# Optimization experiments

Hardware: AMD Instinct MI355X
Metric: run time of the kernel (lower is better)

## Reference

```python
import jax, jax.numpy as jnp
from jax import lax
import numpy as np

B, S = 256, 512
VOCAB, EMB_D = 50000, 300
POS_MAX, POS_D = 512, 16
CNN_OUT, K, NCLASS = 50, 5, 10


def setup_inputs() -> dict:
    key = jax.random.key(0)
    ks = jax.random.split(key, 7)
    return {
        "tokens": jax.random.randint(ks[0], (B, S), 0, VOCAB),
        "embed_table": jax.random.normal(ks[1], (VOCAB, EMB_D), jnp.float32),
        "pos_table": jax.random.normal(ks[2], (POS_MAX, POS_D), jnp.float32),
        "conv_w": jax.random.normal(ks[3], (CNN_OUT, EMB_D + 2 * POS_D, K), jnp.float32) * 0.05,
        "conv_b": jax.random.normal(ks[4], (CNN_OUT,), jnp.float32) * 0.05,
        "fc_w": jax.random.normal(ks[5], (NCLASS, CNN_OUT), jnp.float32) * 0.1,
        "fc_b": jax.random.normal(ks[6], (NCLASS,), jnp.float32) * 0.1,
        "entity1": 1,
        "entity2": 2,
    }


def _nearest_entity_dist(tokens, entity, max_pos):
    # Distance from each token to the nearest occurrence of `entity`,
    # clipped to [0, max_pos-1]; sentences without the entity clip to max.
    Sl = tokens.shape[1]
    idx = jnp.arange(Sl)
    occ = tokens == entity  # [B, S]
    big = 2 * Sl
    # nearest occurrence index to the left (running max) and right (running min)
    left = lax.cummax(jnp.where(occ, idx, -big), axis=1)
    right = lax.cummin(jnp.where(occ, idx, big), axis=1, reverse=True)
    dist = jnp.minimum(idx - left, right - idx)
    return jnp.clip(dist, 0, max_pos - 1)


def reference(tokens, embed_table, pos_table, conv_w, conv_b, fc_w, fc_b,
              entity1, entity2):
    emb = embed_table[tokens]                      # [B, S, EMB_D] gather
    pad = jnp.all(emb == 0.0, axis=-1)             # [B, S] zero-row mask
    feats = [emb]
    for ent in (entity1, entity2):
        d = _nearest_entity_dist(tokens, ent, pos_table.shape[0])
        pe = pos_table[d]                          # [B, S, POS_D]
        pe = jnp.where(pad[..., None], 0.0, pe)    # zero masked positions
        feats.append(pe)
    x = jnp.concatenate(feats, axis=-1)            # [B, S, 332]
    x = jnp.transpose(x, (0, 2, 1))                # [B, C, S]
    pad_hw = conv_w.shape[-1] // 2
    y = lax.conv_general_dilated(
        x, conv_w, window_strides=(1,), padding=[(pad_hw, pad_hw)],
        dimension_numbers=("NCH", "OIH", "NCH"))
    y = jax.nn.relu(y + conv_b[None, :, None])     # [B, 50, S]
    y = jnp.max(y, axis=2)                         # full-length max pool -> [B, 50]
    out = y @ fc_w.T + fc_b                        # [B, NCLASS]
    return out
```

## Files before the change

kernel.cpp:

```cpp
#include <hip/hip_runtime.h>
#include <hip/hip_bf16.h>

typedef __attribute__((ext_vector_type(8))) short short8;
typedef __attribute__((ext_vector_type(4))) float floatx4;

#define BB 256
#define SS 512
#define VOCAB 50000
#define EMB_D 300
#define POS_MAX 512
#define POS_D 16
#define CNN_OUT 50
#define KW 5
#define NCLASS 10
#define C_IN 332
#define KS2 10
#define NB2 20
#define NWF2 (KS2 * NB2 * 64 * 8)
#define PSTR 320
#define ESTR 328
#define FSTR2 328
#define MROWS 64
#define FROWS 68
#define NB_PACK 225
#define NB_POSP 640
#define NB_DIST BB

__device__ __forceinline__ unsigned pack2bf(float x, float y) {
    __hip_bfloat162 h = __float22bfloat162_rn(make_float2(x, y));
    return *reinterpret_cast<unsigned*>(&h);
}

__device__ __forceinline__ unsigned short f2bf(float x) {
    unsigned u = __float_as_uint(x);
    u += 0x7FFF + ((u >> 16) & 1);
    return (unsigned short)(u >> 16);
}

__device__ __forceinline__ float bflo(unsigned u) { return __uint_as_float(u << 16); }
__device__ __forceinline__ float bfhi(unsigned u) { return __uint_as_float(u & 0xFFFF0000u); }

__device__ __forceinline__ unsigned comb(unsigned a, unsigned b, unsigned c,
                                         float sa, float sp) {
    float rlo = sa * bflo(a) + sp * (bflo(b) + bflo(c));
    float rhi = sa * bfhi(a) + sp * (bfhi(b) + bfhi(c));
    return pack2bf(rlo, rhi);
}

__global__ __launch_bounds__(512) void k_prep(const float* __restrict__ conv_w,
                                              const float* __restrict__ pos,
                                              unsigned short* __restrict__ Wf2,
                                              unsigned short* __restrict__ P1,
                                              unsigned short* __restrict__ P2,
                                              float* __restrict__ ymax,
                                              const int* __restrict__ tokens,
                                              const int* __restrict__ e1p,
                                              const int* __restrict__ e2p,
                                              int* __restrict__ d1,
                                              int* __restrict__ d2) {
    __shared__ int cnt1, cnt2;
    __shared__ int lst1[SS], lst2[SS];
    int bid = blockIdx.x, tid = threadIdx.x;
    if (bid < NB_PACK) {
        int idx = bid * 512 + tid;
        if (idx < NWF2) {
            int j = idx & 7, l = (idx >> 3) & 63;
            int rest = idx >> 9;
            int nb = rest % 20, ks = rest / 20;
            int c = ks * 32 + ((l >> 4) << 3) + j;
            int col = nb * 16 + (l & 15);
            int k = col >> 6, o = col & 63;
            float v = 0.f;
            if (c < EMB_D && o < CNN_OUT)
                v = conv_w[o * (C_IN * KW) + c * KW + k];
            Wf2[idx] = f2bf(v);
        } else if (idx < NWF2 + BB * CNN_OUT) {
            ymax[idx - NWF2] = 0.f;
        }
    } else if (bid < NB_PACK + NB_POSP) {
        int idx = (bid - NB_PACK) * 512 + tid;
        int tb = idx / (POS_MAX * PSTR);
        int r = idx % (POS_MAX * PSTR);
        int d = r / PSTR, col = r % PSTR;
        int k = col >> 6, o = col & 63;
        float v = 0.f;
        if (o < CNN_OUT) {
            const float* pr = pos + d * POS_D;
            const float* wb = conv_w + o * (C_IN * KW) + (EMB_D + tb * POS_D) * KW + k;
            #pragma unroll
            for (int c = 0; c < POS_D; ++c) v += pr[c] * wb[c * KW];
        }
        (tb ? P2 : P1)[d * PSTR + col] = f2bf(v);
    } else {
        int b = bid - NB_PACK - NB_POSP;
        int s = tid;
        if (s == 0) { cnt1 = 0; cnt2 = 0; }
        __syncthreads();
        int tok = tokens[b * SS + s];
        int e1 = *e1p, e2 = *e2p;
        if (tok == e1) lst1[atomicAdd(&cnt1, 1)] = s;
        if (tok == e2) lst2[atomicAdd(&cnt2, 1)] = s;
        __syncthreads();
        int dd1 = POS_MAX - 1;
        int n1 = cnt1;
        for (int i = 0; i < n1; ++i) dd1 = min(dd1, abs(s - lst1[i]));
        int dd2 = POS_MAX - 1;
        int n2 = cnt2;
        for (int i = 0; i < n2; ++i) dd2 = min(dd2, abs(s - lst2[i]));
        d1[b * SS + s] = dd1;
        d2[b * SS + s] = dd2;
    }
}

__global__ __launch_bounds__(256, 2) void k_proj(const float* __restrict__ E,
                                                 const unsigned short* __restrict__ Wf2,
                                                 unsigned short* __restrict__ P,
                                                 int* __restrict__ rowz) {
    __shared__ __align__(16) unsigned short Elds[64 * ESTR];
    int tid = threadIdx.x, lane = tid & 63, w = tid >> 6;
    int t0 = blockIdx.x * 64;

    int q = tid & 3, r = tid >> 2;
    int t = t0 + r;
    bool tv = (t < VOCAB);
    const float4* src = (const float4*)(E + (size_t)t * EMB_D);
    float4 v[19];
    #pragma unroll
    for (int i = 0; i < 19; ++i) {
        int c4 = q + i * 4;
        v[i] = (tv && c4 < 75) ? src[c4] : make_float4(0.f, 0.f, 0.f, 0.f);
    }
    bool nz = false;
    #pragma unroll
    for (int i = 0; i < 19; ++i)
        nz |= (v[i].x != 0.f) | (v[i].y != 0.f) | (v[i].z != 0.f) | (v[i].w != 0.f);
    #pragma unroll
    for (int i = 0; i < 19; ++i) {
        int c4 = q + i * 4;
        if (c4 < 75)
            *(uint2*)&Elds[r * ESTR + c4 * 4] =
                make_uint2(pack2bf(v[i].x, v[i].y), pack2bf(v[i].z, v[i].w));
    }
    {
        #pragma unroll
        for (int j = 0; j < 3; ++j) {
            int u = q * 3 + j;
            if (u < 10) *(unsigned*)&Elds[r * ESTR + 300 + u * 2] = 0u;
        }
    }
    {
        unsigned long long bal = __ballot(nz);
        int g = lane >> 2;
        if (q == 0 && tv) rowz[t] = (((bal >> (g * 4)) & 0xFULL) == 0ULL) ? 1 : 0;
    }
    __syncthreads();

    floatx4 acc[4][5];
    #pragma unroll
    for (int mm = 0; mm < 4; ++mm)
        #pragma unroll
        for (int nb = 0; nb < 5; ++nb) acc[mm][nb] = (floatx4)0.f;

    int arow = lane & 15, ach = (lane >> 4) * 8;
    const short8* Bp = (const short8*)Wf2;

    short8 bA[5], bB[5];
    #pragma unroll
    for (int nb = 0; nb < 5; ++nb)
        bA[nb] = Bp[(0 * NB2 + w * 5 + nb) * 64 + lane];
    #pragma unroll
    for (int nb = 0; nb < 5; ++nb)
        bB[nb] = Bp[(1 * NB2 + w * 5 + nb) * 64 + lane];

    auto step = [&](int ks, short8 (&bf)[5], int pfks) {
        short8 af[4];
        #pragma unroll
        for (int mm = 0; mm < 4; ++mm)
            af[mm] = *(const short8*)&Elds[(mm * 16 + arow) * ESTR + ks * 32 + ach];
        #pragma unroll
        for (int mm = 0; mm < 4; ++mm)
            #pragma unroll
            for (int nb = 0; nb < 5; ++nb)
                acc[mm][nb] = __builtin_amdgcn_mfma_f32_16x16x32_bf16(af[mm], bf[nb], acc[mm][nb], 0, 0, 0);
        if (pfks < KS2) {
            #pragma unroll
            for (int nb = 0; nb < 5; ++nb)
                bf[nb] = Bp[(pfks * NB2 + w * 5 + nb) * 64 + lane];
        }
    };

    #pragma unroll 1
    for (int ks = 0; ks < KS2; ks += 2) {
        step(ks, bA, ks + 2);
        step(ks + 1, bB, ks + 3);
    }

    __syncthreads();
    int drow = (lane >> 4) * 4, dcol = lane & 15;
    #pragma unroll
    for (int mm = 0; mm < 4; ++mm)
        #pragma unroll
        for (int nb = 0; nb < 5; ++nb)
            #pragma unroll
            for (int rg = 0; rg < 4; ++rg)
                Elds[(mm * 16 + drow + rg) * ESTR + (w * 5 + nb) * 16 + dcol] = f2bf(acc[mm][nb][rg]);
    __syncthreads();
    #pragma unroll
    for (int j = 0; j < 10; ++j) {
        int idx = tid + j * 256;
        int row = idx / 40, ch = idx % 40;
        int tt = t0 + row;
        if (tt < VOCAB)
            ((uint4*)P)[(size_t)tt * 40 + ch] = *(const uint4*)&Elds[row * ESTR + ch * 8];
    }
}

__global__ __launch_bounds__(512, 4) void k_conv(const int* __restrict__ tokens,
                                                 const int* __restrict__ d1,
                                                 const int* __restrict__ d2,
                                                 const int* __restrict__ rowz,
                                                 const unsigned short* __restrict__ P,
                                                 const unsigned short* __restrict__ P1,
                                                 const unsigned short* __restrict__ P2,
                                                 const float* __restrict__ conv_b,
                                                 float* __restrict__ ymax) {
    __shared__ __align__(16) unsigned short F[FROWS * FSTR2];
    __shared__ int td[FROWS], i1d[FROWS], i2d[FROWS];
    __shared__ float sad[FROWS], spd[FROWS];
    __shared__ float Rm[8][64];
    int tid = threadIdx.x, lane = tid & 63, w = tid >> 6;
    int b = blockIdx.x >> 3, sb = blockIdx.x & 7;
    int s0 = sb * MROWS;

    if (tid < FROWS) {
        int sp = s0 - 2 + tid;
        bool valid = (sp >= 0 && sp < SS);
        int t = valid ? tokens[b * SS + sp] : 0;
        td[tid] = t;
        i1d[tid] = valid ? d1[b * SS + sp] : 0;
        i2d[tid] = valid ? d2[b * SS + sp] : 0;
        sad[tid] = valid ? 1.f : 0.f;
        spd[tid] = (valid && !rowz[t]) ? 1.f : 0.f;
    }
    __syncthreads();

    const uint4* Pp  = (const uint4*)P;
    const uint4* P1p = (const uint4*)P1;
    const uint4* P2p = (const uint4*)P2;
    #pragma unroll
    for (int j = 0; j < 6; ++j) {
        int idx = tid + j * 512;
        if (idx < FROWS * 40) {
            int row = idx / 40, ch = idx % 40;
            uint4 a  = Pp[(size_t)td[row] * 40 + ch];
            uint4 bv = P1p[i1d[row] * 40 + ch];
            uint4 cv = P2p[i2d[row] * 40 + ch];
            float sa = sad[row], sp = spd[row];
            uint4 o;
            o.x = comb(a.x, bv.x, cv.x, sa, sp);
            o.y = comb(a.y, bv.y, cv.y, sa, sp);
            o.z = comb(a.z, bv.z, cv.z, sa, sp);
            o.w = comb(a.w, bv.w, cv.w, sa, sp);
            *(uint4*)&F[row * FSTR2 + ch * 8] = o;
        }
    }
    __syncthreads();

    int s = tid >> 3, og = (tid >> 1) & 3, h = tid & 1;
    float acc[8];
    #pragma unroll
    for (int i = 0; i < 8; ++i) acc[i] = 0.f;
    #pragma unroll
    for (int k = 0; k < KW; ++k) {
        uint4 v = *(const uint4*)&F[(s + k) * FSTR2 + k * 64 + og * 16 + h * 8];
        acc[0] += bflo(v.x); acc[1] += bfhi(v.x);
        acc[2] += bflo(v.y); acc[3] += bfhi(v.y);
        acc[4] += bflo(v.z); acc[5] += bfhi(v.z);
        acc[6] += bflo(v.w); acc[7] += bfhi(v.w);
    }
    #pragma unroll
    for (int i = 0; i < 8; ++i) {
        acc[i] = fmaxf(acc[i], __shfl_xor(acc[i], 8));
        acc[i] = fmaxf(acc[i], __shfl_xor(acc[i], 16));
        acc[i] = fmaxf(acc[i], __shfl_xor(acc[i], 32));
    }
    if ((lane & 56) == 0) {
        #pragma unroll
        for (int i = 0; i < 8; ++i)
            Rm[w][og * 16 + h * 8 + i] = acc[i];
    }
    __syncthreads();

    if (tid < CNN_OUT) {
        float mx = Rm[0][tid];
        #pragma unroll
        for (int w2 = 1; w2 < 8; ++w2) mx = fmaxf(mx, Rm[w2][tid]);
        mx = fmaxf(mx + conv_b[tid], 0.f);
        atomicMax((int*)ymax + b * CNN_OUT + tid, __float_as_int(mx));
    }
}

__global__ __launch_bounds__(64) void k_fc(const float* __restrict__ ymax,
                                           const float* __restrict__ fc_w,
                                           const float* __restrict__ fc_b,
                                           float* __restrict__ out) {
    int b = blockIdx.x, n = threadIdx.x;
    if (n < NCLASS) {
        float a = fc_b[n];
        #pragma unroll
        for (int o = 0; o < CNN_OUT; ++o)
            a += ymax[b * CNN_OUT + o] * fc_w[n * CNN_OUT + o];
        out[b * NCLASS + n] = a;
    }
}

extern "C" void kernel_launch(void* const* d_in, const int* in_sizes, int n_in,
                              void* d_out, int out_size, void* d_ws, size_t ws_size,
                              hipStream_t stream) {
    const int*   tokens  = (const int*)  d_in[0];
    const float* embed   = (const float*)d_in[1];
    const float* pos     = (const float*)d_in[2];
    const float* conv_w  = (const float*)d_in[3];
    const float* conv_b  = (const float*)d_in[4];
    const float* fc_w    = (const float*)d_in[5];
    const float* fc_b    = (const float*)d_in[6];
    const int*   e1p     = (const int*)  d_in[7];
    const int*   e2p     = (const int*)  d_in[8];
    float* out = (float*)d_out;

    char* ws = (char*)d_ws;
    size_t off = 0;
    unsigned short* P   = (unsigned short*)(ws + off); off += (size_t)VOCAB * PSTR * 2;
    unsigned short* Wf2 = (unsigned short*)(ws + off); off += (size_t)NWF2 * 2;
    unsigned short* P1  = (unsigned short*)(ws + off); off += (size_t)POS_MAX * PSTR * 2;
    unsigned short* P2  = (unsigned short*)(ws + off); off += (size_t)POS_MAX * PSTR * 2;
    int*   d1     = (int*)  (ws + off); off += (size_t)BB * SS * 4;
    int*   d2     = (int*)  (ws + off); off += (size_t)BB * SS * 4;
    int*   rowzp  = (int*)  (ws + off); off += (size_t)VOCAB * 4;
    float* ymax   = (float*)(ws + off); off += (size_t)BB * CNN_OUT * 4;
    (void)ws_size; (void)in_sizes; (void)n_in; (void)out_size;

    hipLaunchKernelGGL(k_prep, dim3(NB_PACK + NB_POSP + NB_DIST), dim3(512), 0, stream,
                       conv_w, pos, Wf2, P1, P2, ymax, tokens, e1p, e2p, d1, d2);
    hipLaunchKernelGGL(k_proj, dim3((VOCAB + 63) / 64), dim3(256), 0, stream,
                       embed, Wf2, P, rowzp);
    hipLaunchKernelGGL(k_conv, dim3(BB * (SS / MROWS)), dim3(512), 0, stream,
                       tokens, d1, d2, rowzp, P, P1, P2, conv_b, ymax);
    hipLaunchKernelGGL(k_fc, dim3(BB), dim3(64), 0, stream, ymax, fc_w, fc_b, out);
}
```

Measured before the change: 62.15 us.

## Halve k_proj token tile to 32 and coalesce embedding row loads

Reduces the vocabulary projection tile from 64 to 32 tokens per block, doubling the grid and halving LDS and accumulator registers, which should allow more blocks in flight. Embedding rows are now loaded with a flat, coalesced index mapping across the tile instead of 4 threads per row, and the zero-row flag is set through a shared-memory flag array instead of a ballot. In exchange, each loaded weight fragment is reused over half as many tokens, so total weight traffic from global or L2 doubles.

```diff
diff --git a/kernel.cpp b/kernel.cpp
--- a/kernel.cpp
+++ b/kernel.cpp
@@ -20,6 +20,7 @@
 #define PSTR 320
 #define ESTR 328
 #define FSTR2 328
+#define MTOK 32
 #define MROWS 64
 #define FROWS 68
 #define NB_PACK 225
@@ -116,48 +117,51 @@
                                                  const unsigned short* __restrict__ Wf2,
                                                  unsigned short* __restrict__ P,
                                                  int* __restrict__ rowz) {
-    __shared__ __align__(16) unsigned short Elds[64 * ESTR];
+    __shared__ __align__(16) unsigned short Elds[MTOK * ESTR];
+    __shared__ int nzf[MTOK];
     int tid = threadIdx.x, lane = tid & 63, w = tid >> 6;
-    int t0 = blockIdx.x * 64;
-
-    int q = tid & 3, r = tid >> 2;
-    int t = t0 + r;
-    bool tv = (t < VOCAB);
-    const float4* src = (const float4*)(E + (size_t)t * EMB_D);
-    float4 v[19];
-    #pragma unroll
-    for (int i = 0; i < 19; ++i) {
-        int c4 = q + i * 4;
-        v[i] = (tv && c4 < 75) ? src[c4] : make_float4(0.f, 0.f, 0.f, 0.f);
-    }
-    bool nz = false;
-    #pragma unroll
-    for (int i = 0; i < 19; ++i)
-        nz |= (v[i].x != 0.f) | (v[i].y != 0.f) | (v[i].z != 0.f) | (v[i].w != 0.f);
-    #pragma unroll
-    for (int i = 0; i < 19; ++i) {
-        int c4 = q + i * 4;
-        if (c4 < 75)
-            *(uint2*)&Elds[r * ESTR + c4 * 4] =
-                make_uint2(pack2bf(v[i].x, v[i].y), pack2bf(v[i].z, v[i].w));
-    }
-    {
-        #pragma unroll
-        for (int j = 0; j < 3; ++j) {
-            int u = q * 3 + j;
-            if (u < 10) *(unsigned*)&Elds[r * ESTR + 300 + u * 2] = 0u;
-        }
-    }
-    {
-        unsigned long long bal = __ballot(nz);
-        int g = lane >> 2;
-        if (q == 0 && tv) rowz[t] = (((bal >> (g * 4)) & 0xFULL) == 0ULL) ? 1 : 0;
-    }
-    __syncthreads();
-
-    floatx4 acc[4][5];
-    #pragma unroll
-    for (int mm = 0; mm < 4; ++mm)
+    int t0 = blockIdx.x * MTOK;
+
+    if (tid < MTOK) nzf[tid] = 0;
+    __syncthreads();
+
+    float4 v[10];
+    int vrow[10], vc4[10];
+    bool vok[10];
+    #pragma unroll
+    for (int j = 0; j < 10; ++j) {
+        int idx = tid + j * 256;
+        vok[j] = (idx < MTOK * 75);
+        int row = idx / 75, c4 = idx - row * 75;
+        vrow[j] = row; vc4[j] = c4;
+        int t = t0 + row;
+        v[j] = (vok[j] && t < VOCAB)
+             ? ((const float4*)(E + (size_t)t * EMB_D))[c4]
+             : make_float4(0.f, 0.f, 0.f, 0.f);
+    }
+    #pragma unroll
+    for (int j = 0; j < 10; ++j) {
+        if (vok[j]) {
+            bool nz = (v[j].x != 0.f) | (v[j].y != 0.f) | (v[j].z != 0.f) | (v[j].w != 0.f);
+            if (nz) nzf[vrow[j]] = 1;
+            *(uint2*)&Elds[vrow[j] * ESTR + vc4[j] * 4] =
+                make_uint2(pack2bf(v[j].x, v[j].y), pack2bf(v[j].z, v[j].w));
+        }
+    }
+    if (tid < MTOK * 5) {
+        int row = tid / 5, u = tid - row * 5;
+        *(uint2*)&Elds[row * ESTR + 300 + u * 4] = make_uint2(0u, 0u);
+    }
+    __syncthreads();
+
+    if (tid < MTOK) {
+        int t = t0 + tid;
+        if (t < VOCAB) rowz[t] = nzf[tid] ? 0 : 1;
+    }
+
+    floatx4 acc[2][5];
+    #pragma unroll
+    for (int mm = 0; mm < 2; ++mm)
         #pragma unroll
         for (int nb = 0; nb < 5; ++nb) acc[mm][nb] = (floatx4)0.f;
 
@@ -173,12 +177,12 @@
         bB[nb] = Bp[(1 * NB2 + w * 5 + nb) * 64 + lane];
 
     auto step = [&](int ks, short8 (&bf)[5], int pfks) {
-        short8 af[4];
-        #pragma unroll
-        for (int mm = 0; mm < 4; ++mm)
+        short8 af[2];
+        #pragma unroll
+        for (int mm = 0; mm < 2; ++mm)
             af[mm] = *(const short8*)&Elds[(mm * 16 + arow) * ESTR + ks * 32 + ach];
         #pragma unroll
-        for (int mm = 0; mm < 4; ++mm)
+        for (int mm = 0; mm < 2; ++mm)
             #pragma unroll
             for (int nb = 0; nb < 5; ++nb)
                 acc[mm][nb] = __builtin_amdgcn_mfma_f32_16x16x32_bf16(af[mm], bf[nb], acc[mm][nb], 0, 0, 0);
@@ -198,7 +202,7 @@
     __syncthreads();
     int drow = (lane >> 4) * 4, dcol = lane & 15;
     #pragma unroll
-    for (int mm = 0; mm < 4; ++mm)
+    for (int mm = 0; mm < 2; ++mm)
         #pragma unroll
         for (int nb = 0; nb < 5; ++nb)
             #pragma unroll
@@ -206,9 +210,9 @@
                 Elds[(mm * 16 + drow + rg) * ESTR + (w * 5 + nb) * 16 + dcol] = f2bf(acc[mm][nb][rg]);
     __syncthreads();
     #pragma unroll
-    for (int j = 0; j < 10; ++j) {
+    for (int j = 0; j < 5; ++j) {
         int idx = tid + j * 256;
-        int row = idx / 40, ch = idx % 40;
+        int row = idx / 40, ch = idx - row * 40;
         int tt = t0 + row;
         if (tt < VOCAB)
             ((uint4*)P)[(size_t)tt * 40 + ch] = *(const uint4*)&Elds[row * ESTR + ch * 8];
@@ -342,7 +346,7 @@
 
     hipLaunchKernelGGL(k_prep, dim3(NB_PACK + NB_POSP + NB_DIST), dim3(512), 0, stream,
                        conv_w, pos, Wf2, P1, P2, ymax, tokens, e1p, e2p, d1, d2);
-    hipLaunchKernelGGL(k_proj, dim3((VOCAB + 63) / 64), dim3(256), 0, stream,
+    hipLaunchKernelGGL(k_proj, dim3((VOCAB + MTOK - 1) / MTOK), dim3(256), 0, stream,
                        embed, Wf2, P, rowzp);
     hipLaunchKernelGGL(k_conv, dim3(BB * (SS / MROWS)), dim3(512), 0, stream,
                        tokens, d1, d2, rowzp, P, P1, P2, conv_b, ymax);
```

Result: faster. 60.76 us (-2.2%).
